# Kernel optimization log

Measured on AMD Instinct MI355X. Metric: run time of the kernel, lower is better.

Reference implementation:

```python
import jax, jax.numpy as jnp
import numpy as np

B = 2048          # number of tables (real batch size)
C = 8             # columns per table
D = 768           # hidden size (BERT-base)
TEMP = 0.07       # hp.temp
NEG_FILL = -10.0


def setup_inputs() -> dict:
    key = jax.random.key(0)
    k1, k2, k3 = jax.random.split(key, 3)
    n = B * C
    z = jax.random.normal(k1, (2 * n, D), jnp.float32) * 0.05
    idx = jnp.repeat(jnp.arange(B, dtype=jnp.int32), C)  # contiguous segment ids, as torch.full per table
    query = jax.random.normal(k2, (D, 1), jnp.float32) * 0.05
    attn_temp = jnp.ones((), jnp.float32)
    W = jax.random.normal(k3, (D, D), jnp.float32) * 0.02
    b = jnp.zeros((D,), jnp.float32)
    return {"z": z, "ori_table_indices": idx, "aug_table_indices": idx,
            "query": query, "attn_temp": attn_temp, "W": W, "b": b}


def _attn_pool(z, idx, query, t):
    # scatter-softmax attention pooling over variable-size table segments
    scores = (z @ query)[:, 0] / t                               # [n]
    e = jnp.exp(scores - scores.max())
    denom = jax.ops.segment_sum(e, idx, num_segments=B)[idx]     # [n]
    w = e / (denom + 1e-8)
    return jax.ops.segment_sum(z * w[:, None], idx, num_segments=B)  # [B, D]


def reference(z, ori_table_indices, aug_table_indices, query, attn_temp, W, b):
    n = B * C
    z_ori, z_aug = z[:n], z[n:]
    gx = _attn_pool(z_ori, ori_table_indices, query, attn_temp) @ W.T + b  # [B, D]
    hx = _attn_pool(z_aug, aug_table_indices, query, attn_temp) @ W.T + b  # [B, D]
    f = jnp.concatenate([gx, hx], axis=0)                                  # [2B, D]
    f = f / jnp.linalg.norm(f, axis=1, keepdims=True)
    sim = f @ f.T                                                          # [2B, 2B]
    N = 2 * B
    lab = jnp.concatenate([jnp.arange(B), jnp.arange(B)])
    labels = lab[None, :] == lab[:, None]                                  # [N, N] bool
    potential_pos = (sim > 0.9) & (~labels)
    safe_neg = (~potential_pos) & (~labels)
    # remove diagonal via rotation gather (order of negatives is irrelevant: topk sorts)
    cols = (jnp.arange(N)[:, None] + jnp.arange(1, N)[None, :]) % N        # [N, N-1]
    sim_od = jnp.take_along_axis(sim, cols, axis=1)
    safe_od = jnp.take_along_axis(safe_neg, cols, axis=1)
    # each row's single positive is its paired view at column (i+B) mod N
    pos = jnp.take_along_axis(sim, ((jnp.arange(N) + B) % N)[:, None], axis=1)  # [N, 1]
    neg = jnp.where(safe_od, sim_od, NEG_FILL)
    # data-dependent k; static-shape topk via descending sort + column mask
    k = jnp.maximum(1, jnp.floor(0.5 * jnp.mean(jnp.sum(safe_od, axis=1).astype(jnp.float32))).astype(jnp.int32))
    sneg = -jnp.sort(-neg, axis=1)                                         # descending
    new_neg = jnp.where(jnp.arange(N - 1)[None, :] < k, sneg, NEG_FILL)
    logits = jnp.concatenate([pos, new_neg], axis=1) / TEMP                # [N, N]
    # cross-entropy with target class 0
    loss = jnp.mean(jax.nn.logsumexp(logits, axis=1) - logits[:, 0])
    return loss
```

## Files before the change

kernel.cpp:

```cpp
#include <hip/hip_runtime.h>
#include <hip/hip_bf16.h>
#include <math.h>

#define Bq   2048
#define Cq   8
#define Dq   768
#define NROW 16384
#define NTOT 32768
#define Nq   4096
#define TEMPq 0.07f
#define NKC  96

typedef __attribute__((ext_vector_type(8))) short bf16x8;
typedef __attribute__((ext_vector_type(4))) float f32x4;
typedef __attribute__((ext_vector_type(8))) _Float16 f16x8;

__device__ __hip_bfloat16 g_pooledb[(size_t)Nq * Dq];
__device__ __hip_bfloat16 g_Wb[(size_t)Dq * Dq];
__device__ float          g_f[(size_t)Nq * Dq];
__device__ short          g_fbt[(size_t)NKC * Nq * 8];
__device__ _Float16       g_simh[(size_t)Nq * Nq];
__device__ unsigned int   g_viol;
__device__ float          g_rowloss[Nq];

#define GLDS16(src, dst) __builtin_amdgcn_global_load_lds( \
    (const __attribute__((address_space(1))) void*)(src),  \
    (__attribute__((address_space(3))) void*)(dst), 16, 0, 0)

__global__ __launch_bounds__(256) void prep_kernel(const float* __restrict__ z,
                                                   const float* __restrict__ query,
                                                   const float* __restrict__ attn_temp,
                                                   const float* __restrict__ W) {
    if (blockIdx.x >= 1024) {
        int i = (blockIdx.x - 1024) * 256 + threadIdx.x;
        if (i == 0) g_viol = 0u;
        float4 v = ((const float4*)W)[i];
        short4 o;
        o.x = ((__hip_bfloat16_raw)__float2bfloat16(v.x)).x;
        o.y = ((__hip_bfloat16_raw)__float2bfloat16(v.y)).x;
        o.z = ((__hip_bfloat16_raw)__float2bfloat16(v.z)).x;
        o.w = ((__hip_bfloat16_raw)__float2bfloat16(v.w)).x;
        ((short4*)g_Wb)[i] = o;
        return;
    }
    int seg  = (int)((blockIdx.x * blockDim.x + threadIdx.x) >> 6);
    int lane = threadIdx.x & 63;
    if (seg >= Nq) return;
    int half = seg >> 11;
    int b    = seg & 2047;
    int baseRow = half * NROW + b * Cq;
    float invt = 1.f / attn_temp[0];

    float4 q4[3];
#pragma unroll
    for (int j = 0; j < 3; ++j) q4[j] = *(const float4*)(query + j * 256 + lane * 4);

    float4 v4[Cq][3];
    float s[Cq];
#pragma unroll
    for (int c = 0; c < Cq; ++c) {
        const float* zr = z + (size_t)(baseRow + c) * Dq;
        float acc = 0.f;
#pragma unroll
        for (int j = 0; j < 3; ++j) {
            float4 vz = *(const float4*)(zr + j * 256 + lane * 4);
            v4[c][j] = vz;
            acc += vz.x * q4[j].x + vz.y * q4[j].y + vz.z * q4[j].z + vz.w * q4[j].w;
        }
#pragma unroll
        for (int o = 32; o > 0; o >>= 1) acc += __shfl_xor(acc, o, 64);
        s[c] = acc * invt;
    }
    float m = s[0];
#pragma unroll
    for (int c = 1; c < Cq; ++c) m = fmaxf(m, s[c]);
    float e[Cq], denom = 0.f;
#pragma unroll
    for (int c = 0; c < Cq; ++c) { e[c] = expf(s[c] - m); denom += e[c]; }
    float inv = 1.f / (denom + 1e-8f);
#pragma unroll
    for (int j = 0; j < 3; ++j) {
        float4 acc = {0.f, 0.f, 0.f, 0.f};
#pragma unroll
        for (int c = 0; c < Cq; ++c) {
            acc.x += v4[c][j].x * e[c];
            acc.y += v4[c][j].y * e[c];
            acc.z += v4[c][j].z * e[c];
            acc.w += v4[c][j].w * e[c];
        }
        short4 o;
        o.x = ((__hip_bfloat16_raw)__float2bfloat16(acc.x * inv)).x;
        o.y = ((__hip_bfloat16_raw)__float2bfloat16(acc.y * inv)).x;
        o.z = ((__hip_bfloat16_raw)__float2bfloat16(acc.z * inv)).x;
        o.w = ((__hip_bfloat16_raw)__float2bfloat16(acc.w * inv)).x;
        *(short4*)((short*)g_pooledb + (size_t)seg * Dq + j * 256 + lane * 4) = o;
    }
}

__global__ __launch_bounds__(256) void fw_mfma_kernel(const float* __restrict__ bias) {
    __shared__ short lA[128 * 32];
    __shared__ short lB[128 * 32];
    const int bm = blockIdx.y * 128;
    const int bn = blockIdx.x * 128;

    const int tid  = threadIdx.x;
    const int wave = tid >> 6, lane = tid & 63;
    const int wr = wave >> 1, wc = wave & 1;

    const short* A = (const short*)g_pooledb;
    const short* Bt = (const short*)g_Wb;

    const int c0 = wave * 2, c1 = wave * 2 + 1;
    const int srow = lane >> 2;
    const int scol = (lane & 3) * 8;

    f32x4 acc[4][4];
#pragma unroll
    for (int m = 0; m < 4; ++m)
#pragma unroll
        for (int n = 0; n < 4; ++n) acc[m][n] = (f32x4){0.f, 0.f, 0.f, 0.f};

    for (int k0 = 0; k0 < Dq; k0 += 32) {
        GLDS16(A  + (size_t)(bm + c0 * 16 + srow) * Dq + k0 + scol, lA + c0 * 512);
        GLDS16(A  + (size_t)(bm + c1 * 16 + srow) * Dq + k0 + scol, lA + c1 * 512);
        GLDS16(Bt + (size_t)(bn + c0 * 16 + srow) * Dq + k0 + scol, lB + c0 * 512);
        GLDS16(Bt + (size_t)(bn + c1 * 16 + srow) * Dq + k0 + scol, lB + c1 * 512);
        __syncthreads();

        bf16x8 af[4], bfr[4];
#pragma unroll
        for (int m = 0; m < 4; ++m) {
            int row = wr * 64 + m * 16 + (lane & 15);
            af[m] = *(const bf16x8*)(lA + row * 32 + (lane >> 4) * 8);
        }
#pragma unroll
        for (int n = 0; n < 4; ++n) {
            int row = wc * 64 + n * 16 + (lane & 15);
            bfr[n] = *(const bf16x8*)(lB + row * 32 + (lane >> 4) * 8);
        }
#pragma unroll
        for (int m = 0; m < 4; ++m)
#pragma unroll
            for (int n = 0; n < 4; ++n)
                acc[m][n] = __builtin_amdgcn_mfma_f32_16x16x32_bf16(af[m], bfr[n], acc[m][n], 0, 0, 0);
        __syncthreads();
    }

#pragma unroll
    for (int m = 0; m < 4; ++m) {
        int rowb = bm + wr * 64 + m * 16 + (lane >> 4) * 4;
#pragma unroll
        for (int n = 0; n < 4; ++n) {
            int col = bn + wc * 64 + n * 16 + (lane & 15);
            float bc = bias[col];
#pragma unroll
            for (int j = 0; j < 4; ++j)
                g_f[(size_t)(rowb + j) * Dq + col] = acc[m][n][j] + bc;
        }
    }
}

__global__ __launch_bounds__(256) void normalize_kernel() {
    __shared__ short rowbuf[16][776];
    const int tid = threadIdx.x;
    const int wave = tid >> 6, lane = tid & 63;
    const int r0 = blockIdx.x * 16;

    for (int rr = wave; rr < 16; rr += 4) {
        int row = r0 + rr;
        float v[12];
        float ss = 0.f;
#pragma unroll
        for (int j = 0; j < 12; ++j) { v[j] = g_f[(size_t)row * Dq + j * 64 + lane]; ss += v[j] * v[j]; }
#pragma unroll
        for (int o = 32; o > 0; o >>= 1) ss += __shfl_xor(ss, o, 64);
        float rn = 1.f / sqrtf(ss);
#pragma unroll
        for (int j = 0; j < 12; ++j)
            rowbuf[rr][j * 64 + lane] = ((__hip_bfloat16_raw)__float2bfloat16(v[j] * rn)).x;
    }
    __syncthreads();
#pragma unroll
    for (int i = 0; i < 6; ++i) {
        int idx = i * 256 + tid;
        int ch = idx >> 4;
        int r  = idx & 15;
        bf16x8 val = *(const bf16x8*)&rowbuf[r][ch * 8];
        *(bf16x8*)&g_fbt[((size_t)ch * Nq + r0 + r) * 8] = val;
    }
}

#define STAGE_SIM(b, kt_) do {                                                          \
    _Pragma("unroll")                                                                   \
    for (int i = 0; i < 4; ++i) {                                                       \
        GLDS16(fbt + ((size_t)((kt_) * 8 + wave) * Nq + bm + i * 64 + lane) * 8,        \
               As + ((b) * 2048 + wave * 256 + i * 64) * 8);                            \
        GLDS16(fbt + ((size_t)((kt_) * 8 + wave) * Nq + bn + i * 64 + lane) * 8,        \
               Bs + ((b) * 2048 + wave * 256 + i * 64) * 8);                            \
    }                                                                                   \
} while (0)

__global__ __launch_bounds__(512) void sim_mfma_kernel() {
    extern __shared__ short smem[];
    short* As = smem;
    short* Bs = smem + 32768;

    const int tid  = threadIdx.x;
    const int wave = tid >> 6, lane = tid & 63;
    const int wm = wave >> 2, wn = wave & 3;
    const int bm = blockIdx.y * 256, bn = blockIdx.x * 256;
    const short* fbt = g_fbt;

    f32x4 acc[8][4];
#pragma unroll
    for (int mi = 0; mi < 8; ++mi)
#pragma unroll
        for (int ni = 0; ni < 4; ++ni) acc[mi][ni] = (f32x4){0.f, 0.f, 0.f, 0.f};

    STAGE_SIM(0, 0);

#pragma unroll 1
    for (int kt = 0; kt < 12; ++kt) {
        const int cur = kt & 1;
        if (kt < 11) {
            STAGE_SIM(cur ^ 1, kt + 1);
            asm volatile("s_waitcnt vmcnt(8)" ::: "memory");
        } else {
            asm volatile("s_waitcnt vmcnt(0)" ::: "memory");
        }
        __builtin_amdgcn_s_barrier();
        __builtin_amdgcn_sched_barrier(0);

#pragma unroll
        for (int ks = 0; ks < 2; ++ks) {
            bf16x8 af[8], bfr[4];
            const int kc = (ks * 4 + (lane >> 4)) * 256;
#pragma unroll
            for (int mi = 0; mi < 8; ++mi)
                af[mi] = *(const bf16x8*)(As + (cur * 2048 + kc + wm * 128 + mi * 16 + (lane & 15)) * 8);
#pragma unroll
            for (int ni = 0; ni < 4; ++ni)
                bfr[ni] = *(const bf16x8*)(Bs + (cur * 2048 + kc + wn * 64 + ni * 16 + (lane & 15)) * 8);
            __builtin_amdgcn_s_setprio(1);
#pragma unroll
            for (int mi = 0; mi < 8; ++mi)
#pragma unroll
                for (int ni = 0; ni < 4; ++ni)
                    acc[mi][ni] = __builtin_amdgcn_mfma_f32_16x16x32_bf16(af[mi], bfr[ni], acc[mi][ni], 0, 0, 0);
            __builtin_amdgcn_s_setprio(0);
        }
        __builtin_amdgcn_sched_barrier(0);
        __builtin_amdgcn_s_barrier();
    }

    int vio = 0;
#pragma unroll
    for (int mi = 0; mi < 8; ++mi) {
        int rowb = bm + wm * 128 + mi * 16 + (lane >> 4) * 4;
#pragma unroll
        for (int ni = 0; ni < 4; ++ni) {
            int col = bn + wn * 64 + ni * 16 + (lane & 15);
#pragma unroll
            for (int j = 0; j < 4; ++j) {
                float x = acc[mi][ni][j];
                g_simh[(size_t)(rowb + j) * Nq + col] = (_Float16)x;
                vio += (x > 0.9f) && ((((rowb + j) ^ col) & 2047) != 0);
            }
        }
    }
#pragma unroll
    for (int o = 32; o > 0; o >>= 1) vio += __shfl_xor(vio, o, 64);
    if (lane == 0 && vio > 0) atomicAdd(&g_viol, (unsigned int)vio);
}

__global__ __launch_bounds__(256) void lse_kernel() {
    const int row_id = (int)((blockIdx.x * blockDim.x + threadIdx.x) >> 6);
    const int lane = threadIdx.x & 63;
    const _Float16* row = g_simh + (size_t)row_id * Nq;
    const int labi = row_id & 2047;
    const float invT = 1.0f / TEMPq;

    long long total = (long long)Nq * 4094LL - (long long)g_viol;
    int k = (int)(total / 8192LL);
    if (k < 1) k = 1;

    float v[64];
    float mx = -1e30f, mn = 1e30f;
    int cnt = 0;
#pragma unroll
    for (int q = 0; q < 8; ++q) {
        int j0 = q * 512 + lane * 8;
        f16x8 x8 = *(const f16x8*)(row + j0);
#pragma unroll
        for (int s = 0; s < 8; ++s) {
            int jj = q * 8 + s;
            int j  = j0 + s;
            float xv = (float)x8[s];
            bool sf = (xv <= 0.9f) && (((j ^ labi) & 2047) != 0);
            float val = sf ? xv : -2.0f;
            v[jj] = val;
            mx = fmaxf(mx, val);
            mn = fminf(mn, sf ? xv : 2.0f);
            cnt += (int)__popcll(__ballot(sf));
        }
    }
#pragma unroll
    for (int o = 32; o > 0; o >>= 1) {
        mx = fmaxf(mx, __shfl_xor(mx, o, 64));
        mn = fminf(mn, __shfl_xor(mn, o, 64));
    }

    const float pos = (float)row[(row_id + Bq) & (Nq - 1)];
    const float mxs = (cnt > 0) ? mx : -10.0f;
    const float ml  = fmaxf(pos, mxs) * invT;

    float lo = mn - 1e-3f, hi = mx;
    int c_hi = 0;
    const bool need = (cnt > k);
    if (need) {
        for (int it = 0; it < 12; ++it) {
            float mid = 0.5f * (lo + hi);
            int c = 0;
#pragma unroll
            for (int jj = 0; jj < 64; ++jj)
                c += (int)__popcll(__ballot(v[jj] > mid));
            if (c > k) lo = mid; else { hi = mid; c_hi = c; }
        }
    }

    float shi = 0.f, st = 0.f; int nt = 0;
#pragma unroll
    for (int jj = 0; jj < 64; ++jj) {
        float x = v[jj];
        float ev = __expf(x * invT - ml);
        if (!need)       { if (x > -1.5f) shi += ev; }
        else if (x > hi) { shi += ev; }
        else if (x > lo) { st += ev; nt++; }
    }
#pragma unroll
    for (int o = 32; o > 0; o >>= 1) {
        shi += __shfl_xor(shi, o, 64);
        st  += __shfl_xor(st,  o, 64);
        nt  += __shfl_xor(nt,  o, 64);
    }
    if (lane == 0) {
        float S = __expf(pos * invT - ml) + shi;
        if (need && c_hi < k && nt > 0)
            S += st * (float)(k - c_hi) / (float)nt;
        g_rowloss[row_id] = (logf(S) + ml) - pos * invT;
    }
}

__global__ __launch_bounds__(256) void loss_kernel(float* __restrict__ out) {
    float s = 0.f;
    for (int i = threadIdx.x; i < Nq; i += 256) s += g_rowloss[i];
    __shared__ float sm[256];
    sm[threadIdx.x] = s; __syncthreads();
    for (int o = 128; o > 0; o >>= 1) {
        if (threadIdx.x < o) sm[threadIdx.x] += sm[threadIdx.x + o];
        __syncthreads();
    }
    if (threadIdx.x == 0) out[0] = sm[0] / (float)Nq;
}

extern "C" void kernel_launch(void* const* d_in, const int* in_sizes, int n_in,
                              void* d_out, int out_size, void* d_ws, size_t ws_size,
                              hipStream_t stream) {
    const float* z         = (const float*)d_in[0];
    const float* query     = (const float*)d_in[3];
    const float* attn_temp = (const float*)d_in[4];
    const float* W         = (const float*)d_in[5];
    const float* bias      = (const float*)d_in[6];
    float* out = (float*)d_out;

    prep_kernel<<<1024 + (Dq * Dq / 4) / 256, 256, 0, stream>>>(z, query, attn_temp, W);
    fw_mfma_kernel<<<dim3(Dq / 128, Nq / 128), 256, 0, stream>>>(bias);
    normalize_kernel<<<Nq / 16, 256, 0, stream>>>();
    sim_mfma_kernel<<<dim3(16, 16), 512, 131072, stream>>>();
    lse_kernel<<<Nq / 4, 256, 0, stream>>>();
    loss_kernel<<<1, 256, 0, stream>>>(out);
}
```

Before: 116.3 us.

## Stage sim tile through LDS for coalesced stores, swizzle blocks, fuse final reduction

The sim GEMM epilogue now writes its fp16 tile into shared memory and then stores it to global in 16-byte coalesced rows, replacing the scattered 2-byte stores. Block indices are remapped with a swizzle so consecutive blocks land on different XCD-friendly tiles. The separate loss reduction kernel is removed: each LSE row atomically adds into a global accumulator, and the last block writes the mean. This saves a launch and cuts store inefficiency, at the cost of float atomic contention and a nondeterministic summation order.

```diff
diff --git a/kernel.cpp b/kernel.cpp
--- a/kernel.cpp
+++ b/kernel.cpp
@@ -21,7 +21,8 @@
 __device__ short          g_fbt[(size_t)NKC * Nq * 8];
 __device__ _Float16       g_simh[(size_t)Nq * Nq];
 __device__ unsigned int   g_viol;
-__device__ float          g_rowloss[Nq];
+__device__ float          g_lossacc;
+__device__ unsigned int   g_done;
 
 #define GLDS16(src, dst) __builtin_amdgcn_global_load_lds( \
     (const __attribute__((address_space(1))) void*)(src),  \
@@ -33,7 +34,7 @@
                                                    const float* __restrict__ W) {
     if (blockIdx.x >= 1024) {
         int i = (blockIdx.x - 1024) * 256 + threadIdx.x;
-        if (i == 0) g_viol = 0u;
+        if (i == 0) { g_viol = 0u; g_lossacc = 0.f; g_done = 0u; }
         float4 v = ((const float4*)W)[i];
         short4 o;
         o.x = ((__hip_bfloat16_raw)__float2bfloat16(v.x)).x;
@@ -208,7 +209,9 @@
     const int tid  = threadIdx.x;
     const int wave = tid >> 6, lane = tid & 63;
     const int wm = wave >> 2, wn = wave & 3;
-    const int bm = blockIdx.y * 256, bn = blockIdx.x * 256;
+    const int bid = blockIdx.x;
+    const int sw  = (bid & 7) * 32 + (bid >> 3);
+    const int bm = (sw >> 4) * 256, bn = (sw & 15) * 256;
     const short* fbt = g_fbt;
 
     f32x4 acc[8][4];
@@ -254,26 +257,41 @@
     }
 
     int vio = 0;
+    short* ct = smem;
 #pragma unroll
     for (int mi = 0; mi < 8; ++mi) {
-        int rowb = bm + wm * 128 + mi * 16 + (lane >> 4) * 4;
+        int rloc = wm * 128 + mi * 16 + (lane >> 4) * 4;
 #pragma unroll
         for (int ni = 0; ni < 4; ++ni) {
-            int col = bn + wn * 64 + ni * 16 + (lane & 15);
+            int cloc = wn * 64 + ni * 16 + (lane & 15);
 #pragma unroll
             for (int j = 0; j < 4; ++j) {
                 float x = acc[mi][ni][j];
-                g_simh[(size_t)(rowb + j) * Nq + col] = (_Float16)x;
-                vio += (x > 0.9f) && ((((rowb + j) ^ col) & 2047) != 0);
+                vio += (x > 0.9f) && ((((bm + rloc + j) ^ (bn + cloc)) & 2047) != 0);
+                union { _Float16 h; short s; } cv; cv.h = (_Float16)x;
+                ct[(rloc + j) * 256 + cloc] = cv.s;
             }
         }
     }
 #pragma unroll
     for (int o = 32; o > 0; o >>= 1) vio += __shfl_xor(vio, o, 64);
     if (lane == 0 && vio > 0) atomicAdd(&g_viol, (unsigned int)vio);
-}
-
-__global__ __launch_bounds__(256) void lse_kernel() {
+    __syncthreads();
+
+    const int g  = lane >> 3, s8 = lane & 7;
+#pragma unroll
+    for (int p = 0; p < 4; ++p) {
+        int r = p * 64 + wave * 8 + g;
+#pragma unroll
+        for (int it = 0; it < 4; ++it) {
+            int c = it * 64 + s8 * 8;
+            bf16x8 val = *(const bf16x8*)&ct[r * 256 + c];
+            *(bf16x8*)&g_simh[(size_t)(bm + r) * Nq + bn + c] = val;
+        }
+    }
+}
+
+__global__ __launch_bounds__(256) void lse_kernel(float* __restrict__ out) {
     const int row_id = (int)((blockIdx.x * blockDim.x + threadIdx.x) >> 6);
     const int lane = threadIdx.x & 63;
     const _Float16* row = g_simh + (size_t)row_id * Nq;
@@ -347,20 +365,17 @@
         float S = __expf(pos * invT - ml) + shi;
         if (need && c_hi < k && nt > 0)
             S += st * (float)(k - c_hi) / (float)nt;
-        g_rowloss[row_id] = (logf(S) + ml) - pos * invT;
-    }
-}
-
-__global__ __launch_bounds__(256) void loss_kernel(float* __restrict__ out) {
-    float s = 0.f;
-    for (int i = threadIdx.x; i < Nq; i += 256) s += g_rowloss[i];
-    __shared__ float sm[256];
-    sm[threadIdx.x] = s; __syncthreads();
-    for (int o = 128; o > 0; o >>= 1) {
-        if (threadIdx.x < o) sm[threadIdx.x] += sm[threadIdx.x + o];
-        __syncthreads();
-    }
-    if (threadIdx.x == 0) out[0] = sm[0] / (float)Nq;
+        atomicAdd(&g_lossacc, (logf(S) + ml) - pos * invT);
+    }
+    __syncthreads();
+    if (threadIdx.x == 0) {
+        __threadfence();
+        unsigned int done = atomicAdd(&g_done, 1u);
+        if (done == gridDim.x - 1) {
+            __threadfence();
+            out[0] = atomicAdd(&g_lossacc, 0.0f) / (float)Nq;
+        }
+    }
 }
 
 extern "C" void kernel_launch(void* const* d_in, const int* in_sizes, int n_in,
@@ -376,7 +391,6 @@
     prep_kernel<<<1024 + (Dq * Dq / 4) / 256, 256, 0, stream>>>(z, query, attn_temp, W);
     fw_mfma_kernel<<<dim3(Dq / 128, Nq / 128), 256, 0, stream>>>(bias);
     normalize_kernel<<<Nq / 16, 256, 0, stream>>>();
-    sim_mfma_kernel<<<dim3(16, 16), 512, 131072, stream>>>();
-    lse_kernel<<<Nq / 4, 256, 0, stream>>>();
-    loss_kernel<<<1, 256, 0, stream>>>(out);
-}
+    sim_mfma_kernel<<<256, 512, 131072, stream>>>();
+    lse_kernel<<<Nq / 4, 256, 0, stream>>>(out);
+}
```

Measured after the change: 165.7 us. 1.43x slower.
